# Kernel tuning notes

Measured on AMD Instinct MI355X. Metric: run time of the kernel, lower is better.

Reference implementation:

```python
import jax, jax.numpy as jnp
import numpy as np

EPS = 1e-12  # torch F.normalize default eps


def setup_inputs() -> dict:
    key = jax.random.key(0)
    ks = jax.random.split(key, 7)
    dim, heads = 128, 8
    b, c, s, h, w = 2, dim, 3, 128, 128
    sc = 1.0 / np.sqrt(dim)
    return {
        "x": jax.random.normal(ks[0], (b, c, s, h, w), dtype=jnp.float32),
        "Wq": jax.random.normal(ks[1], (dim, dim), dtype=jnp.float32) * sc,
        "Wk": jax.random.normal(ks[2], (dim, dim), dtype=jnp.float32) * sc,
        "Wv": jax.random.normal(ks[3], (dim, dim), dtype=jnp.float32) * sc,
        "Wp": jax.random.normal(ks[4], (dim, dim), dtype=jnp.float32) * sc,
        "bp": jax.random.normal(ks[5], (dim,), dtype=jnp.float32) * 0.01,
        "rescale": jnp.ones((heads, 1, 1), dtype=jnp.float32),
    }


def _l2norm(t):
    # torch F.normalize(p=2, dim=-1): t / max(||t||, eps)
    n = jnp.sqrt(jnp.sum(t * t, axis=-1, keepdims=True))
    return t / jnp.maximum(n, EPS)


def reference(x, Wq, Wk, Wv, Wp, bp, rescale):
    b, c, s, h, w = x.shape
    heads = rescale.shape[0]
    d = c // heads
    n = h * w * s
    # [b,c,s,h,w] -> [b,h,w,s,c] -> [b, n, c]
    xt = jnp.transpose(x, (0, 3, 4, 2, 1)).reshape(b, n, c)
    # torch Linear: y = x @ W.T
    q = xt @ Wq.T
    k = xt @ Wk.T
    v = xt @ Wv.T
    # [b,n,heads,d] -> [b,heads,d,n] (channel attention: tokens along last axis)
    def to_heads(t):
        return jnp.transpose(t.reshape(b, n, heads, d), (0, 2, 3, 1))
    q, k, v = to_heads(q), to_heads(k), to_heads(v)
    q = _l2norm(q)
    k = _l2norm(k)
    # attn: [b,heads,d,d] = k @ q^T over token axis n
    attn = jnp.einsum('bhdn,bhen->bhde', k, q)
    attn = attn * rescale  # rescale broadcasts as [heads,1,1]
    attn = jax.nn.softmax(attn, axis=-1)
    out = jnp.einsum('bhde,bhen->bhdn', attn, v)  # [b,heads,d,n]
    # [b,heads,d,n] -> [b,n,heads*d]
    out = jnp.transpose(out, (0, 3, 1, 2)).reshape(b, n, c)
    out = out @ Wp.T + bp
    # [b,n,c] -> [b,h,w,s,c] -> [b,h,w,c,s] -> [b,c,s,h,w]
    out = out.reshape(b, h, w, s, c)
    out = jnp.transpose(out, (0, 1, 2, 4, 3))
    out = jnp.transpose(out, (0, 3, 4, 1, 2))
    return out
```

## Files before the change

### kernel.cpp

```cpp
#include <hip/hip_runtime.h>
#include <hip/hip_bf16.h>

typedef __bf16 bf16_t;
typedef __bf16 bf16x8 __attribute__((ext_vector_type(8)));
typedef float f32x4 __attribute__((ext_vector_type(4)));

#define NTOK 49152
#define CDIM 128
#define CHUNKS 192
#define KT 256
#define STEPS 8

__device__ inline f32x4 mfma16(bf16x8 a, bf16x8 b, f32x4 c) {
  return __builtin_amdgcn_mfma_f32_16x16x32_bf16(a, b, c, 0, 0, 0);
}

__global__ __launch_bounds__(256) void k1_gram(const float* __restrict__ x,
                                               float* __restrict__ part) {
  const int blk = blockIdx.x;
  const int b = blk / CHUNKS, chunk = blk % CHUNKS;
  const float* Xb = x + (size_t)b * CDIM * NTOK;
  const int tid = threadIdx.x, wave = tid >> 6, lane = tid & 63;
  const int r = lane & 15, quad = lane >> 4;

  __shared__ __align__(16) bf16_t tile[2][128 * 32];

  const int sch = tid >> 1, shalf = tid & 1;
  const float* gsrc = Xb + (size_t)sch * NTOK + chunk * KT + shalf * 16;

  f32x4 st[4];
#define STAGE_LOAD(step)                                   \
  {                                                        \
    const float* p_ = gsrc + (step) * 32;                  \
    st[0] = *(const f32x4*)(p_ + 0);                       \
    st[1] = *(const f32x4*)(p_ + 4);                       \
    st[2] = *(const f32x4*)(p_ + 8);                       \
    st[3] = *(const f32x4*)(p_ + 12);                      \
  }
#define STAGE_WRITE(buf)                                              \
  {                                                                   \
    bf16_t* t_ = &tile[buf][0];                                       \
    _Pragma("unroll")                                                 \
    for (int j_ = 0; j_ < 16; ++j_) {                                 \
      const int tok_ = shalf * 16 + j_;                               \
      const int c16_ = ((sch >> 4) << 6) + ((tok_ >> 3) << 4) + (sch & 15); \
      t_[c16_ * 8 + (tok_ & 7)] = (bf16_t)st[j_ >> 2][j_ & 3];        \
    }                                                                 \
  }

  f32x4 acc[2][8];
#pragma unroll
  for (int t = 0; t < 2; ++t)
#pragma unroll
    for (int j = 0; j < 8; ++j) acc[t][j] = (f32x4){0.f, 0.f, 0.f, 0.f};

  STAGE_LOAD(0);
  STAGE_WRITE(0);
  __syncthreads();

  for (int k = 0; k < STEPS; ++k) {
    const int buf = k & 1;
    if (k + 1 < STEPS) STAGE_LOAD(k + 1);
    bf16x8 frag[8];
#pragma unroll
    for (int g = 0; g < 8; ++g)
      frag[g] = *(const bf16x8*)&tile[buf][(g * 64 + lane) * 8];
    bf16x8 a0, a1;
    if (wave == 0)      { a0 = frag[0]; a1 = frag[1]; }
    else if (wave == 1) { a0 = frag[2]; a1 = frag[3]; }
    else if (wave == 2) { a0 = frag[4]; a1 = frag[5]; }
    else                { a0 = frag[6]; a1 = frag[7]; }
#pragma unroll
    for (int j = 0; j < 8; ++j) {
      acc[0][j] = mfma16(a0, frag[j], acc[0][j]);
      acc[1][j] = mfma16(a1, frag[j], acc[1][j]);
    }
    if (k + 1 < STEPS) STAGE_WRITE(1 - buf);
    __syncthreads();
  }
#undef STAGE_LOAD
#undef STAGE_WRITE

  float* pb = part + ((size_t)(b * CHUNKS + chunk) << 14);
#pragma unroll
  for (int t = 0; t < 2; ++t) {
#pragma unroll
    for (int j = 0; j < 8; ++j) {
#pragma unroll
      for (int reg = 0; reg < 4; ++reg) {
        const int row = wave * 32 + t * 16 + quad * 4 + reg;
        const int col = 16 * j + r;
        pb[row * 128 + col] = acc[t][j][reg];
      }
    }
  }
}

__global__ __launch_bounds__(256) void k2a_reduce(const float* __restrict__ part,
                                                  float* __restrict__ part2) {
  const int gid = blockIdx.x * 256 + threadIdx.x;
  const int e4 = gid & 4095, sl = (gid >> 12) & 7, b = gid >> 15;
  const float* p = part + ((size_t)(b * CHUNKS + sl * 24) << 14) + e4 * 4;
  f32x4 s = (f32x4){0.f, 0.f, 0.f, 0.f};
#pragma unroll 8
  for (int i = 0; i < 24; ++i) s += *(const f32x4*)(p + ((size_t)i << 14));
  *(f32x4*)(part2 + ((size_t)(b * 8 + sl) << 14) + e4 * 4) = s;
}

__global__ __launch_bounds__(256) void k2b_reduce(const float* __restrict__ part2,
                                                  float* __restrict__ S) {
  const int gid = blockIdx.x * 256 + threadIdx.x;
  const int e4 = gid & 4095, b = gid >> 12;
  f32x4 s = (f32x4){0.f, 0.f, 0.f, 0.f};
#pragma unroll
  for (int sl = 0; sl < 8; ++sl)
    s += *(const f32x4*)(part2 + ((size_t)(b * 8 + sl) << 14) + e4 * 4);
  *(f32x4*)(S + ((size_t)b << 14) + e4 * 4) = s;
}

__global__ __launch_bounds__(256) void k3_t(const float* __restrict__ S,
                                            const float* __restrict__ Wk,
                                            const float* __restrict__ Wq,
                                            float* __restrict__ Tm) {
  const int idx = blockIdx.x * 256 + threadIdx.x;
  const int j = idx & 127, i = (idx >> 7) & 127, t = (idx >> 14) & 1, b = idx >> 15;
  const f32x4* w4 = (const f32x4*)((t ? Wq : Wk) + i * 128);
  const f32x4* s4 = (const f32x4*)(S + (b << 14) + j * 128);
  float s = 0.f;
#pragma unroll 8
  for (int q = 0; q < 32; ++q) {
    const f32x4 a = w4[q], v = s4[q];
    s += a[0] * v[0] + a[1] * v[1] + a[2] * v[2] + a[3] * v[3];
  }
  Tm[idx] = s;
}

__global__ __launch_bounds__(256) void k3_attn(const float* __restrict__ Tm,
                                               const float* __restrict__ Wk,
                                               const float* __restrict__ Wq,
                                               const float* __restrict__ resc,
                                               float* __restrict__ attn) {
  const int blk = blockIdx.x;
  const int b = blk >> 3, h = blk & 7;
  const int tid = threadIdx.x, d = tid >> 4, e = tid & 15;
  const float* Tk = Tm + (size_t)(b * 2 + 0) * 16384;
  const float* Tq = Tm + (size_t)(b * 2 + 1) * 16384;

  const float* tkrow = Tk + (h * 16 + d) * 128;
  const float* wqrow = Wq + (h * 16 + e) * 128;
  float g = 0.f;
#pragma unroll 4
  for (int c = 0; c < 128; ++c) g += tkrow[c] * wqrow[c];

  __shared__ float sqk[16], sqq[16];
  if (e == 0) {
    const float* wkrow = Wk + (h * 16 + d) * 128;
    float s = 0.f;
    for (int c = 0; c < 128; ++c) s += tkrow[c] * wkrow[c];
    sqk[d] = s;
  }
  if (d == 0) {
    const float* tqrow = Tq + (h * 16 + e) * 128;
    float s = 0.f;
    for (int c = 0; c < 128; ++c) s += tqrow[c] * wqrow[c];
    sqq[e] = s;
  }
  __syncthreads();

  const float nk = fmaxf(sqrtf(fmaxf(sqk[d], 0.f)), 1e-12f);
  const float nq = fmaxf(sqrtf(fmaxf(sqq[e], 0.f)), 1e-12f);
  float pre = g / (nk * nq) * resc[h];

  float mx = pre;
#pragma unroll
  for (int m = 1; m < 16; m <<= 1) mx = fmaxf(mx, __shfl_xor(mx, m, 64));
  const float p = expf(pre - mx);
  float sum = p;
#pragma unroll
  for (int m = 1; m < 16; m <<= 1) sum += __shfl_xor(sum, m, 64);
  attn[blk * 256 + tid] = p / sum;
}

__global__ __launch_bounds__(256) void k3_p(const float* __restrict__ attn,
                                            const float* __restrict__ Wp,
                                            const float* __restrict__ Wv,
                                            bf16_t* __restrict__ Phi) {
  const int blk = blockIdx.x;
  const int b = blk >> 7, rrow = blk & 127;
  const int tid = threadIdx.x;
  __shared__ float M[128];
  if (tid < 128) {
    const int h = tid >> 4, e = tid & 15;
    const float* A = attn + (size_t)(b * 8 + h) * 256;
    const float* wp = Wp + rrow * 128 + h * 16;
    float m = 0.f;
#pragma unroll
    for (int d = 0; d < 16; ++d) m += wp[d] * A[d * 16 + e];
    M[tid] = m;
  }
  __syncthreads();
  if (tid < 128) {
    const int c = tid;
    float p = 0.f;
#pragma unroll 4
    for (int j = 0; j < 128; ++j) p += M[j] * Wv[j * 128 + c];
    Phi[((size_t)b << 14) + rrow * 128 + c] = (bf16_t)p;
  }
}

__global__ __launch_bounds__(256) void k4_out(const float* __restrict__ x,
                                              const bf16_t* __restrict__ Phi,
                                              const float* __restrict__ bp,
                                              float* __restrict__ out) {
  const int blk = blockIdx.x;
  const int b = blk / 768, tg = blk % 768;
  const float* Xb = x + (size_t)b * CDIM * NTOK;
  const bf16_t* Ph = Phi + ((size_t)b << 14);
  float* Ob = out + (size_t)b * CDIM * NTOK;
  const int tid = threadIdx.x, wave = tid >> 6, lane = tid & 63;
  const int r = lane & 15, quad = lane >> 4;
  const int tok0 = tg * 64;

  __shared__ __align__(16) bf16_t tile[128 * 64];

  {
    const int sch = tid >> 1, shalf = tid & 1;
    const float* p = Xb + (size_t)sch * NTOK + tok0 + shalf * 32;
    f32x4 st[8];
#pragma unroll
    for (int q = 0; q < 8; ++q) st[q] = *(const f32x4*)(p + q * 4);
    const int chunk_hi = ((sch >> 5) << 8) + (((sch >> 3) & 3) << 4);
    const int ei = sch & 7;
#pragma unroll
    for (int j = 0; j < 32; ++j) {
      const int tok = shalf * 32 + j;
      const int chunk = chunk_hi + ((tok >> 4) << 6) + (tok & 15);
      tile[chunk * 8 + ei] = (bf16_t)st[j >> 2][j & 3];
    }
  }
  __syncthreads();

  f32x4 acc[8];
#pragma unroll
  for (int m = 0; m < 8; ++m) acc[m] = (f32x4){0.f, 0.f, 0.f, 0.f};

#pragma unroll
  for (int step = 0; step < 4; ++step) {
    const bf16x8 bfr = *(const bf16x8*)&tile[(step * 256 + wave * 64 + lane) * 8];
#pragma unroll
    for (int m = 0; m < 8; ++m) {
      const bf16x8 ah = *(const bf16x8*)(Ph + (16 * m + r) * 128 + step * 32 + quad * 8);
      acc[m] = mfma16(ah, bfr, acc[m]);
    }
  }

  const int wtok = tok0 + wave * 16;
#pragma unroll
  for (int m = 0; m < 8; ++m) {
#pragma unroll
    for (int reg = 0; reg < 4; ++reg) {
      const int row = m * 16 + quad * 4 + reg;
      Ob[(size_t)row * NTOK + wtok + r] = acc[m][reg] + bp[row];
    }
  }
}

extern "C" void kernel_launch(void* const* d_in, const int* in_sizes, int n_in,
                              void* d_out, int out_size, void* d_ws, size_t ws_size,
                              hipStream_t stream) {
  const float* x    = (const float*)d_in[0];
  const float* Wq   = (const float*)d_in[1];
  const float* Wk   = (const float*)d_in[2];
  const float* Wv   = (const float*)d_in[3];
  const float* Wp   = (const float*)d_in[4];
  const float* bp   = (const float*)d_in[5];
  const float* resc = (const float*)d_in[6];
  float* out = (float*)d_out;

  char* ws = (char*)d_ws;
  float*  S    = (float*)(ws + 0);
  float*  Tm   = (float*)(ws + 131072);
  float*  attn = (float*)(ws + 393216);
  bf16_t* Phi  = (bf16_t*)(ws + 409600);
  float* part  = (float*)d_out;
  float* part2 = (float*)((char*)d_out + 25165824);

  k1_gram<<<2 * CHUNKS, 256, 0, stream>>>(x, part);
  k2a_reduce<<<256, 256, 0, stream>>>(part, part2);
  k2b_reduce<<<32, 256, 0, stream>>>(part2, S);
  k3_t<<<256, 256, 0, stream>>>(S, Wk, Wq, Tm);
  k3_attn<<<16, 256, 0, stream>>>(Tm, Wk, Wq, resc, attn);
  k3_p<<<256, 256, 0, stream>>>(attn, Wp, Wv, Phi);
  k4_out<<<1536, 256, 0, stream>>>(x, Phi, bp, out);
}
```

Baseline: 179.5 us.

## Fuse final reduce, T projection and attention into one kernel; rebalance gram chunks

Merges the second-stage reduction, the W·S projection and the attention/softmax kernels into a single 16-block kernel that keeps S and the per-head T rows in shared memory. This removes two launches and the global round trips of S and Tm. The gram stage now uses 256 chunks of 192 tokens, so 512 blocks instead of 384 fill the GPU better. Partial sums move to the workspace when it is large enough. The trade-off is that the fused kernel runs only 16 blocks, each redundantly reducing a full 128x128 S from eight partials.

```diff
diff --git a/kernel.cpp b/kernel.cpp
--- a/kernel.cpp
+++ b/kernel.cpp
@@ -7,9 +7,9 @@
 
 #define NTOK 49152
 #define CDIM 128
-#define CHUNKS 192
-#define KT 256
-#define STEPS 8
+#define CHUNKS 256
+#define KT 192
+#define STEPS 6
 
 __device__ inline f32x4 mfma16(bf16x8 a, bf16x8 b, f32x4 c) {
   return __builtin_amdgcn_mfma_f32_16x16x32_bf16(a, b, c, 0, 0, 0);
@@ -18,7 +18,7 @@
 __global__ __launch_bounds__(256) void k1_gram(const float* __restrict__ x,
                                                float* __restrict__ part) {
   const int blk = blockIdx.x;
-  const int b = blk / CHUNKS, chunk = blk % CHUNKS;
+  const int b = blk >> 8, chunk = blk & 255;
   const float* Xb = x + (size_t)b * CDIM * NTOK;
   const int tid = threadIdx.x, wave = tid >> 6, lane = tid & 63;
   const int r = lane & 15, quad = lane >> 4;
@@ -100,69 +100,82 @@
                                                   float* __restrict__ part2) {
   const int gid = blockIdx.x * 256 + threadIdx.x;
   const int e4 = gid & 4095, sl = (gid >> 12) & 7, b = gid >> 15;
-  const float* p = part + ((size_t)(b * CHUNKS + sl * 24) << 14) + e4 * 4;
+  const float* p = part + ((size_t)(b * CHUNKS + sl * 32) << 14) + e4 * 4;
   f32x4 s = (f32x4){0.f, 0.f, 0.f, 0.f};
 #pragma unroll 8
-  for (int i = 0; i < 24; ++i) s += *(const f32x4*)(p + ((size_t)i << 14));
+  for (int i = 0; i < 32; ++i) s += *(const f32x4*)(p + ((size_t)i << 14));
   *(f32x4*)(part2 + ((size_t)(b * 8 + sl) << 14) + e4 * 4) = s;
 }
 
-__global__ __launch_bounds__(256) void k2b_reduce(const float* __restrict__ part2,
-                                                  float* __restrict__ S) {
-  const int gid = blockIdx.x * 256 + threadIdx.x;
-  const int e4 = gid & 4095, b = gid >> 12;
-  f32x4 s = (f32x4){0.f, 0.f, 0.f, 0.f};
-#pragma unroll
-  for (int sl = 0; sl < 8; ++sl)
-    s += *(const f32x4*)(part2 + ((size_t)(b * 8 + sl) << 14) + e4 * 4);
-  *(f32x4*)(S + ((size_t)b << 14) + e4 * 4) = s;
-}
-
-__global__ __launch_bounds__(256) void k3_t(const float* __restrict__ S,
-                                            const float* __restrict__ Wk,
-                                            const float* __restrict__ Wq,
-                                            float* __restrict__ Tm) {
-  const int idx = blockIdx.x * 256 + threadIdx.x;
-  const int j = idx & 127, i = (idx >> 7) & 127, t = (idx >> 14) & 1, b = idx >> 15;
-  const f32x4* w4 = (const f32x4*)((t ? Wq : Wk) + i * 128);
-  const f32x4* s4 = (const f32x4*)(S + (b << 14) + j * 128);
-  float s = 0.f;
+__global__ __launch_bounds__(256) void k3_ta(const float* __restrict__ part2,
+                                             const float* __restrict__ Wk,
+                                             const float* __restrict__ Wq,
+                                             const float* __restrict__ resc,
+                                             float* __restrict__ attn) {
+  const int blk = blockIdx.x;
+  const int b = blk >> 3, h = blk & 7;
+  const int tid = threadIdx.x;
+  __shared__ float Sl[128 * 132];
+  __shared__ float Tkl[16 * 132];
+  __shared__ float Tql[16 * 132];
+
+  for (int idx = tid; idx < 16384; idx += 256) {
+    float s = 0.f;
+#pragma unroll
+    for (int sl = 0; sl < 8; ++sl)
+      s += part2[((size_t)(b * 8 + sl) << 14) + idx];
+    Sl[(idx >> 7) * 132 + (idx & 127)] = s;
+  }
+  __syncthreads();
+
+  const int c = tid & 127, hl = tid >> 7;
+#pragma unroll
+  for (int t = 0; t < 2; ++t) {
+    const float* W = (t ? Wq : Wk);
+    float* Tl = (t ? Tql : Tkl);
+    const f32x4* s4 = (const f32x4*)(Sl + c * 132);
+#pragma unroll
+    for (int rep = 0; rep < 8; ++rep) {
+      const int d = rep * 2 + hl;
+      const f32x4* w4 = (const f32x4*)(W + (h * 16 + d) * 128);
+      float v = 0.f;
+#pragma unroll 8
+      for (int q = 0; q < 32; ++q) {
+        const f32x4 a = w4[q], s = s4[q];
+        v += a[0] * s[0] + a[1] * s[1] + a[2] * s[2] + a[3] * s[3];
+      }
+      Tl[d * 132 + c] = v;
+    }
+  }
+  __syncthreads();
+
+  const int e = tid & 15, d = tid >> 4;
+  const f32x4* tk4 = (const f32x4*)(Tkl + d * 132);
+  const f32x4* wq4 = (const f32x4*)(Wq + (h * 16 + e) * 128);
+  float g = 0.f;
 #pragma unroll 8
   for (int q = 0; q < 32; ++q) {
-    const f32x4 a = w4[q], v = s4[q];
-    s += a[0] * v[0] + a[1] * v[1] + a[2] * v[2] + a[3] * v[3];
-  }
-  Tm[idx] = s;
-}
-
-__global__ __launch_bounds__(256) void k3_attn(const float* __restrict__ Tm,
-                                               const float* __restrict__ Wk,
-                                               const float* __restrict__ Wq,
-                                               const float* __restrict__ resc,
-                                               float* __restrict__ attn) {
-  const int blk = blockIdx.x;
-  const int b = blk >> 3, h = blk & 7;
-  const int tid = threadIdx.x, d = tid >> 4, e = tid & 15;
-  const float* Tk = Tm + (size_t)(b * 2 + 0) * 16384;
-  const float* Tq = Tm + (size_t)(b * 2 + 1) * 16384;
-
-  const float* tkrow = Tk + (h * 16 + d) * 128;
-  const float* wqrow = Wq + (h * 16 + e) * 128;
-  float g = 0.f;
-#pragma unroll 4
-  for (int c = 0; c < 128; ++c) g += tkrow[c] * wqrow[c];
+    const f32x4 a = tk4[q], w = wq4[q];
+    g += a[0] * w[0] + a[1] * w[1] + a[2] * w[2] + a[3] * w[3];
+  }
 
   __shared__ float sqk[16], sqq[16];
   if (e == 0) {
-    const float* wkrow = Wk + (h * 16 + d) * 128;
+    const f32x4* wk4 = (const f32x4*)(Wk + (h * 16 + d) * 128);
     float s = 0.f;
-    for (int c = 0; c < 128; ++c) s += tkrow[c] * wkrow[c];
+    for (int q = 0; q < 32; ++q) {
+      const f32x4 a = tk4[q], w = wk4[q];
+      s += a[0] * w[0] + a[1] * w[1] + a[2] * w[2] + a[3] * w[3];
+    }
     sqk[d] = s;
   }
   if (d == 0) {
-    const float* tqrow = Tq + (h * 16 + e) * 128;
+    const f32x4* tq4 = (const f32x4*)(Tql + e * 132);
     float s = 0.f;
-    for (int c = 0; c < 128; ++c) s += tqrow[c] * wqrow[c];
+    for (int q = 0; q < 32; ++q) {
+      const f32x4 a = tq4[q], w = wq4[q];
+      s += a[0] * w[0] + a[1] * w[1] + a[2] * w[2] + a[3] * w[3];
+    }
     sqq[e] = s;
   }
   __syncthreads();
@@ -278,18 +291,23 @@
   float* out = (float*)d_out;
 
   char* ws = (char*)d_ws;
-  float*  S    = (float*)(ws + 0);
-  float*  Tm   = (float*)(ws + 131072);
-  float*  attn = (float*)(ws + 393216);
-  bf16_t* Phi  = (bf16_t*)(ws + 409600);
-  float* part  = (float*)d_out;
-  float* part2 = (float*)((char*)d_out + 25165824);
+  float*  attn = (float*)(ws + 0);
+  bf16_t* Phi  = (bf16_t*)(ws + 16384);
+  const size_t part_off  = 1 << 20;
+  const size_t part_sz   = (size_t)2 * CHUNKS * 16384 * sizeof(float);
+  const size_t part2_off = part_off + part_sz;
+  float* part, * part2;
+  if (ws_size >= part2_off + (1 << 20)) {
+    part  = (float*)(ws + part_off);
+    part2 = (float*)(ws + part2_off);
+  } else {
+    part  = (float*)d_out;
+    part2 = (float*)((char*)d_out + part_sz);
+  }
 
   k1_gram<<<2 * CHUNKS, 256, 0, stream>>>(x, part);
   k2a_reduce<<<256, 256, 0, stream>>>(part, part2);
-  k2b_reduce<<<32, 256, 0, stream>>>(part2, S);
-  k3_t<<<256, 256, 0, stream>>>(S, Wk, Wq, Tm);
-  k3_attn<<<16, 256, 0, stream>>>(Tm, Wk, Wq, resc, attn);
+  k3_ta<<<16, 256, 0, stream>>>(part2, Wk, Wq, resc, attn);
   k3_p<<<256, 256, 0, stream>>>(attn, Wp, Wv, Phi);
   k4_out<<<1536, 256, 0, stream>>>(x, Phi, bp, out);
 }
```

Result: slower. 215.6 us (+20.1%).
